# Kernel optimization log

Hardware: AMD Instinct MI355X
Metric: run time of the kernel (lower is better)

## Reference

```python
import jax, jax.numpy as jnp
import numpy as np

B, C, NX, NY = 8, 128, 256, 256
N = 32768

def setup_inputs() -> dict:
    key = jax.random.key(0)
    k1, k2 = jax.random.split(key)
    x = jax.random.normal(k1, (B, C, NX, NY), dtype=jnp.float32)
    coords = jax.random.uniform(k2, (B, N, 2), dtype=jnp.float32)
    return {"x": x, "coords": coords}

def reference(x, coords):
    b, c, nx, ny = x.shape
    # Match torch: scale by (dim-1), clamp to [0, dim], floor to int (nearest-lower gather).
    px = jnp.clip(coords[:, :, 1] * (nx - 1), 0, nx).astype(jnp.int32)  # (b, n)
    py = jnp.clip(coords[:, :, 0] * (ny - 1), 0, ny).astype(jnp.int32)  # (b, n)
    # Direct per-batch gather: out[b, c, n] = x[b, c, px[b,n], py[b,n]]
    flat_idx = px * ny + py                                             # (b, n)
    x_flat = x.reshape(b, c, nx * ny)                                   # (b, c, nx*ny)
    out = jnp.take_along_axis(x_flat, flat_idx[:, None, :], axis=2)     # (b, c, n)
    return out
```

## Files before the change

### kernel.cpp

```cpp
#include <hip/hip_runtime.h>
#include <hip/hip_bf16.h>

#define B_  8
#define C_  128
#define NX_ 256
#define NY_ 256
#define N_  32768
#define PLANE_ (NX_ * NY_)
#define XT_BYTES ((size_t)B_ * PLANE_ * C_ * 4)
#define BM_WORDS_PER_B (PLANE_ / 32)
#define BM_BYTES ((size_t)B_ * BM_WORDS_PER_B * 4)

__device__ __forceinline__ int sample_idx(const float* __restrict__ coords, int b, int n) {
    const float2 cc = *reinterpret_cast<const float2*>(coords + ((size_t)b * N_ + n) * 2);
    const int px = (int)fminf(fmaxf(cc.y * (float)(NX_ - 1), 0.0f), (float)NX_);
    const int py = (int)fminf(fmaxf(cc.x * (float)(NY_ - 1), 0.0f), (float)NY_);
    return min(px * NY_ + py, PLANE_ - 1);
}

__global__ __launch_bounds__(256) void mark_kernel(const float* __restrict__ coords,
                                                   unsigned* __restrict__ bm) {
    const int n = blockIdx.x * 256 + threadIdx.x;
    const int b = blockIdx.y;
    const int idx = sample_idx(coords, b, n);
    atomicOr(&bm[b * BM_WORDS_PER_B + (idx >> 5)], 1u << (idx & 31));
}

__global__ __launch_bounds__(256) void transpose_kernel(const float* __restrict__ x,
                                                        const unsigned* __restrict__ bm,
                                                        float* __restrict__ xT) {
    __shared__ float tile[32][129];
    const int bid = blockIdx.x;
    const int b   = bid & 7;
    const int p0  = (bid >> 3) << 5;
    const int t   = threadIdx.x;

    const float* __restrict__ xb = x + (size_t)b * C_ * PLANE_;
    const int pl = t & 31, cr = t >> 5;
    #pragma unroll
    for (int r = 0; r < 16; ++r) {
        const int c = r * 8 + cr;
        tile[pl][c] = xb[(size_t)c * PLANE_ + p0 + pl];
    }
    __syncthreads();

    float* __restrict__ xTb = xT + (size_t)b * PLANE_ * C_;
    const int c = t & 127, ph = t >> 7;
    #pragma unroll
    for (int r = 0; r < 16; ++r) {
        const int p = r * 2 + ph;
        const unsigned w = bm[b * BM_WORDS_PER_B + ((p0 + p) >> 5)];
        if (w & (1u << ((p0 + p) & 31)))
            xTb[(size_t)(p0 + p) * C_ + c] = tile[p][c];
    }
}

__global__ __launch_bounds__(256) void gather_kernel(const float* __restrict__ xT,
                                                     const float* __restrict__ coords,
                                                     float* __restrict__ out) {
    __shared__ float smp[64][130];
    __shared__ int   sidx[64];
    const int bid = blockIdx.x;
    const int b   = bid & 7;
    const int n0  = (bid >> 3) << 6;
    const int t   = threadIdx.x;

    if (t < 64) sidx[t] = sample_idx(coords, b, n0 + t);
    __syncthreads();

    const float* __restrict__ xTb = xT + (size_t)b * PLANE_ * C_;
    const int g = t & 63, sr = t >> 6;
    #pragma unroll
    for (int r = 0; r < 16; ++r) {
        const int s = r * 4 + sr;
        const float2 v = *reinterpret_cast<const float2*>(&xTb[(size_t)sidx[s] * C_ + 2 * g]);
        *reinterpret_cast<float2*>(&smp[s][2 * g]) = v;
    }
    __syncthreads();

    float* __restrict__ ob = out + (size_t)b * C_ * N_ + n0;
    const int s = t & 63, ch = t >> 6;
    #pragma unroll
    for (int r = 0; r < 32; ++r) {
        const int c = r * 4 + ch;
        __builtin_nontemporal_store(smp[s][c], ob + (size_t)c * N_ + s);
    }
}

__global__ __launch_bounds__(256) void fallback_kernel(const float* __restrict__ x,
                                                       const float* __restrict__ coords,
                                                       float* __restrict__ out) {
    const int bid  = blockIdx.x;
    const int b    = bid & 7;
    const int rem  = bid >> 3;
    const int cg   = rem >> 7;
    const int nblk = rem & 127;
    const int n  = nblk * 256 + threadIdx.x;
    const int c0 = cg * 8;
    const int idx = sample_idx(coords, b, n);
    const float* __restrict__ xb = x + ((size_t)b * C_ + c0) * PLANE_ + idx;
    float* __restrict__ ob = out + ((size_t)b * C_ + c0) * N_ + n;
    #pragma unroll
    for (int i = 0; i < 8; ++i)
        __builtin_nontemporal_store(xb[(size_t)i * PLANE_], ob + (size_t)i * N_);
}

extern "C" void kernel_launch(void* const* d_in, const int* in_sizes, int n_in,
                              void* d_out, int out_size, void* d_ws, size_t ws_size,
                              hipStream_t stream) {
    const float* x      = (const float*)d_in[0];
    const float* coords = (const float*)d_in[1];
    float* out          = (float*)d_out;

    if (ws_size >= XT_BYTES + BM_BYTES) {
        float*    xT = (float*)d_ws;
        unsigned* bm = (unsigned*)((char*)d_ws + XT_BYTES);
        hipMemsetAsync(bm, 0, BM_BYTES, stream);
        mark_kernel<<<dim3(N_ / 256, B_), 256, 0, stream>>>(coords, bm);
        transpose_kernel<<<B_ * (PLANE_ / 32), 256, 0, stream>>>(x, bm, xT);
        gather_kernel<<<B_ * (N_ / 64), 256, 0, stream>>>(xT, coords, out);
    } else {
        fallback_kernel<<<B_ * 16 * 128, 256, 0, stream>>>(x, coords, out);
    }
}
```

Measured before the change: 461.3 us.

## Replace transpose-and-gather pipeline with direct per-channel gather plus L2 prefetch

Drops the bitmap marking, sparse transpose and workspace gather kernels and instead gathers each channel plane directly from x in one kernel. Each block handles 1024 samples across 64 channels, issuing coalesced dummy vector loads a few channels ahead to pull the plane into cache before the random gathers. This removes the intermediate transposed write and re-read, at the cost of uncoalesced scattered reads and a small grid.

New measurement: 548.6 us. 18.9% more time.

```diff
diff --git a/kernel.cpp b/kernel.cpp
--- a/kernel.cpp
+++ b/kernel.cpp
@@ -1,5 +1,4 @@
 #include <hip/hip_runtime.h>
-#include <hip/hip_bf16.h>
 
 #define B_  8
 #define C_  128
@@ -7,9 +6,8 @@
 #define NY_ 256
 #define N_  32768
 #define PLANE_ (NX_ * NY_)
-#define XT_BYTES ((size_t)B_ * PLANE_ * C_ * 4)
-#define BM_WORDS_PER_B (PLANE_ / 32)
-#define BM_BYTES ((size_t)B_ * BM_WORDS_PER_B * 4)
+
+typedef float f32x4 __attribute__((ext_vector_type(4)));
 
 __device__ __forceinline__ int sample_idx(const float* __restrict__ coords, int b, int n) {
     const float2 cc = *reinterpret_cast<const float2*>(coords + ((size_t)b * N_ + n) * 2);
@@ -18,91 +16,41 @@
     return min(px * NY_ + py, PLANE_ - 1);
 }
 
-__global__ __launch_bounds__(256) void mark_kernel(const float* __restrict__ coords,
-                                                   unsigned* __restrict__ bm) {
-    const int n = blockIdx.x * 256 + threadIdx.x;
-    const int b = blockIdx.y;
-    const int idx = sample_idx(coords, b, n);
-    atomicOr(&bm[b * BM_WORDS_PER_B + (idx >> 5)], 1u << (idx & 31));
-}
-
-__global__ __launch_bounds__(256) void transpose_kernel(const float* __restrict__ x,
-                                                        const unsigned* __restrict__ bm,
-                                                        float* __restrict__ xT) {
-    __shared__ float tile[32][129];
+__global__ __launch_bounds__(256, 2) void gather_direct(const float* __restrict__ x,
+                                                        const float* __restrict__ coords,
+                                                        float* __restrict__ out) {
     const int bid = blockIdx.x;
     const int b   = bid & 7;
-    const int p0  = (bid >> 3) << 5;
+    const int cg  = (bid >> 3) & 1;
+    const int nt  = bid >> 4;
+    const int n0  = nt << 10;
     const int t   = threadIdx.x;
 
-    const float* __restrict__ xb = x + (size_t)b * C_ * PLANE_;
-    const int pl = t & 31, cr = t >> 5;
+    int idx[4];
     #pragma unroll
-    for (int r = 0; r < 16; ++r) {
-        const int c = r * 8 + cr;
-        tile[pl][c] = xb[(size_t)c * PLANE_ + p0 + pl];
+    for (int k = 0; k < 4; ++k) idx[k] = sample_idx(coords, b, n0 + t + 256 * k);
+
+    const float* __restrict__ xb = x + ((size_t)b * C_ + (size_t)cg * 64) * PLANE_;
+    float* __restrict__ ob = out + ((size_t)b * C_ + (size_t)cg * 64) * N_ + n0;
+
+    const float* __restrict__ pfb = xb + nt * 2048 + t * 8;
+
+    #pragma unroll 2
+    for (int c = 0; c < 64; ++c) {
+        const int cpf = (c + 3 < 64) ? (c + 3) : 63;
+        {
+            const f32x4 p0 = *reinterpret_cast<const f32x4*>(pfb + (size_t)cpf * PLANE_);
+            const f32x4 p1 = *reinterpret_cast<const f32x4*>(pfb + (size_t)cpf * PLANE_ + 4);
+            asm volatile("" :: "v"(p0), "v"(p1));
+        }
+        const float* __restrict__ xp = xb + (size_t)c * PLANE_;
+        float v[4];
+        #pragma unroll
+        for (int k = 0; k < 4; ++k) v[k] = xp[idx[k]];
+        #pragma unroll
+        for (int k = 0; k < 4; ++k)
+            __builtin_nontemporal_store(v[k], ob + (size_t)c * N_ + t + 256 * k);
     }
-    __syncthreads();
-
-    float* __restrict__ xTb = xT + (size_t)b * PLANE_ * C_;
-    const int c = t & 127, ph = t >> 7;
-    #pragma unroll
-    for (int r = 0; r < 16; ++r) {
-        const int p = r * 2 + ph;
-        const unsigned w = bm[b * BM_WORDS_PER_B + ((p0 + p) >> 5)];
-        if (w & (1u << ((p0 + p) & 31)))
-            xTb[(size_t)(p0 + p) * C_ + c] = tile[p][c];
-    }
-}
-
-__global__ __launch_bounds__(256) void gather_kernel(const float* __restrict__ xT,
-                                                     const float* __restrict__ coords,
-                                                     float* __restrict__ out) {
-    __shared__ float smp[64][130];
-    __shared__ int   sidx[64];
-    const int bid = blockIdx.x;
-    const int b   = bid & 7;
-    const int n0  = (bid >> 3) << 6;
-    const int t   = threadIdx.x;
-
-    if (t < 64) sidx[t] = sample_idx(coords, b, n0 + t);
-    __syncthreads();
-
-    const float* __restrict__ xTb = xT + (size_t)b * PLANE_ * C_;
-    const int g = t & 63, sr = t >> 6;
-    #pragma unroll
-    for (int r = 0; r < 16; ++r) {
-        const int s = r * 4 + sr;
-        const float2 v = *reinterpret_cast<const float2*>(&xTb[(size_t)sidx[s] * C_ + 2 * g]);
-        *reinterpret_cast<float2*>(&smp[s][2 * g]) = v;
-    }
-    __syncthreads();
-
-    float* __restrict__ ob = out + (size_t)b * C_ * N_ + n0;
-    const int s = t & 63, ch = t >> 6;
-    #pragma unroll
-    for (int r = 0; r < 32; ++r) {
-        const int c = r * 4 + ch;
-        __builtin_nontemporal_store(smp[s][c], ob + (size_t)c * N_ + s);
-    }
-}
-
-__global__ __launch_bounds__(256) void fallback_kernel(const float* __restrict__ x,
-                                                       const float* __restrict__ coords,
-                                                       float* __restrict__ out) {
-    const int bid  = blockIdx.x;
-    const int b    = bid & 7;
-    const int rem  = bid >> 3;
-    const int cg   = rem >> 7;
-    const int nblk = rem & 127;
-    const int n  = nblk * 256 + threadIdx.x;
-    const int c0 = cg * 8;
-    const int idx = sample_idx(coords, b, n);
-    const float* __restrict__ xb = x + ((size_t)b * C_ + c0) * PLANE_ + idx;
-    float* __restrict__ ob = out + ((size_t)b * C_ + c0) * N_ + n;
-    #pragma unroll
-    for (int i = 0; i < 8; ++i)
-        __builtin_nontemporal_store(xb[(size_t)i * PLANE_], ob + (size_t)i * N_);
 }
 
 extern "C" void kernel_launch(void* const* d_in, const int* in_sizes, int n_in,
@@ -111,15 +59,5 @@
     const float* x      = (const float*)d_in[0];
     const float* coords = (const float*)d_in[1];
     float* out          = (float*)d_out;
-
-    if (ws_size >= XT_BYTES + BM_BYTES) {
-        float*    xT = (float*)d_ws;
-        unsigned* bm = (unsigned*)((char*)d_ws + XT_BYTES);
-        hipMemsetAsync(bm, 0, BM_BYTES, stream);
-        mark_kernel<<<dim3(N_ / 256, B_), 256, 0, stream>>>(coords, bm);
-        transpose_kernel<<<B_ * (PLANE_ / 32), 256, 0, stream>>>(x, bm, xT);
-        gather_kernel<<<B_ * (N_ / 64), 256, 0, stream>>>(xT, coords, out);
-    } else {
-        fallback_kernel<<<B_ * 16 * 128, 256, 0, stream>>>(x, coords, out);
-    }
+    gather_direct<<<B_ * 2 * (N_ / 1024), 256, 0, stream>>>(x, coords, out);
 }
```
